# Optimization experiments

Measured on AMD Instinct MI355X. Metric: run time of the kernel, lower is better.

The kernel has to match this reference:

```python
import jax, jax.numpy as jnp
import numpy as np

EPS = 1e-12  # torch F.normalize eps

def _l2norm(v, axis):
    n = jnp.sqrt(jnp.sum(v * v, axis=axis, keepdims=True))
    return v / jnp.maximum(n, EPS)

def setup_inputs() -> dict:
    key = jax.random.key(0)
    k1, k2, k3 = jax.random.split(key, 3)
    B, M, D, K = 32, 2048, 1024, 64
    init_sc = 1.0 / np.sqrt(D)
    x = jax.random.normal(k1, (B, M, D), dtype=jnp.float32)
    W = init_sc * jax.random.normal(k2, (K, D), dtype=jnp.float32)          # fc1.weight
    centroids = init_sc * jax.random.normal(k3, (K, D), dtype=jnp.float32)  # self.centeroids
    return {"x": x, "W": W, "centroids": centroids}

def reference(x, W, centroids):
    # x: [B, M, D] frame features; W, centroids: [K, D]
    x = _l2norm(x, axis=-1)                                   # per-frame L2 normalize
    logits = jnp.einsum('bmd,kd->bmk', x, W)                  # fc1 (no bias)
    a = jax.nn.softmax(logits, axis=-1)                       # soft assignment [B, M, K]
    # vlad[b,k,:] = sum_m a[b,m,k] * (x[b,m,:] - centroids[k,:])
    #            = (A^T X)[b,k,:] - (sum_m a[b,m,k]) * centroids[k,:]
    vlad = jnp.einsum('bmk,bmd->bkd', a, x) - a.sum(axis=1)[..., None] * centroids
    vlad = _l2norm(vlad, axis=-1)                             # intra-normalization per cluster
    v = vlad.reshape(vlad.shape[0], -1)                       # [B, K*D]
    return _l2norm(v, axis=-1)                                # global L2 normalize
```

## Files before the change

### kernel.cpp

```cpp
#include <hip/hip_runtime.h>
#include <math.h>


#define NB 32
#define NM 2048
#define ND 1024
#define NK 64

typedef float f32x4 __attribute__((ext_vector_type(4)));
typedef short s16x4 __attribute__((ext_vector_type(4)));
typedef short s16x8 __attribute__((ext_vector_type(8)));

static constexpr float EPS_ = 1e-12f;

__device__ __forceinline__ short f2bf(float f) {
    union { float f; unsigned u; } v; v.f = f;
    unsigned r = v.u + 0x7fffu + ((v.u >> 16) & 1u);
    return (short)(r >> 16);
}

__global__ __launch_bounds__(256) void nv1_logits_softmax(
    const float* __restrict__ x, const float* __restrict__ W,
    short* __restrict__ aT, float* __restrict__ asum)
{
    const int b = blockIdx.y, mt = blockIdx.x;
    const int tid  = threadIdx.x;
    const int w    = tid >> 6, lane = tid & 63, g = lane >> 4, c = lane & 15;
    const int wm   = w >> 1, wk = w & 1;

    __shared__ union {
        struct { short Xs[64][72]; short Ws[64][72]; } st;
        float Ls[64][68];
    } sm;
    __shared__ float red[64][16];
    __shared__ float inv_l[64];
    __shared__ float asum_l[64];

    f32x4 acc[2][2] = {};
    float sq[4] = {0.f, 0.f, 0.f, 0.f};

    const int sr = tid >> 4;
    const int sc = tid & 15;
    const float* xb = x + ((size_t)b * NM + (size_t)mt * 64) * ND;

    for (int d0 = 0; d0 < ND; d0 += 64) {
        __syncthreads();
        #pragma unroll
        for (int i = 0; i < 4; ++i) {
            const int r = sr + 16 * i;
            const float4 xv = *(const float4*)(xb + (size_t)r * ND + d0 + sc * 4);
            const float4 wv = *(const float4*)(W  + (size_t)r * ND + d0 + sc * 4);
            sq[i] += xv.x*xv.x + xv.y*xv.y + xv.z*xv.z + xv.w*xv.w;
            s16x4 xh, wh;
            xh[0]=f2bf(xv.x); xh[1]=f2bf(xv.y); xh[2]=f2bf(xv.z); xh[3]=f2bf(xv.w);
            wh[0]=f2bf(wv.x); wh[1]=f2bf(wv.y); wh[2]=f2bf(wv.z); wh[3]=f2bf(wv.w);
            *(s16x4*)&sm.st.Xs[r][sc * 4] = xh;
            *(s16x4*)&sm.st.Ws[r][sc * 4] = wh;
        }
        __syncthreads();
        #pragma unroll
        for (int s = 0; s < 2; ++s) {
            s16x8 af[2], bf[2];
            #pragma unroll
            for (int f = 0; f < 2; ++f) {
                af[f] = *(const s16x8*)&sm.st.Xs[wm*32 + f*16 + c][s*32 + g*8];
                bf[f] = *(const s16x8*)&sm.st.Ws[wk*32 + f*16 + c][s*32 + g*8];
            }
            #pragma unroll
            for (int fm = 0; fm < 2; ++fm)
                #pragma unroll
                for (int fk = 0; fk < 2; ++fk)
                    acc[fm][fk] = __builtin_amdgcn_mfma_f32_16x16x32_bf16(
                        af[fm], bf[fk], acc[fm][fk], 0, 0, 0);
        }
    }
    __syncthreads();
    #pragma unroll
    for (int i = 0; i < 4; ++i) red[sr + 16*i][sc] = sq[i];
    #pragma unroll
    for (int fm = 0; fm < 2; ++fm)
        #pragma unroll
        for (int fk = 0; fk < 2; ++fk)
            #pragma unroll
            for (int r = 0; r < 4; ++r)
                sm.Ls[wm*32 + fm*16 + g*4 + r][wk*32 + fk*16 + c] = acc[fm][fk][r];
    __syncthreads();
    if (tid < 64) {
        float s = 0.f;
        #pragma unroll
        for (int i = 0; i < 16; ++i) s += red[tid][i];
        inv_l[tid]  = 1.f / fmaxf(sqrtf(s), EPS_);
        asum_l[tid] = 0.f;
    }
    __syncthreads();

    const int row = tid >> 2, q = tid & 3;
    const float iv = inv_l[row];
    float e[16];
    float mx = -3.0e38f;
    #pragma unroll
    for (int j = 0; j < 16; ++j) { e[j] = sm.Ls[row][q*16 + j] * iv; mx = fmaxf(mx, e[j]); }
    mx = fmaxf(mx, __shfl_xor(mx, 1, 64));
    mx = fmaxf(mx, __shfl_xor(mx, 2, 64));
    float smv = 0.f;
    #pragma unroll
    for (int j = 0; j < 16; ++j) { e[j] = __expf(e[j] - mx); smv += e[j]; }
    smv += __shfl_xor(smv, 1, 64);
    smv += __shfl_xor(smv, 2, 64);
    const float rs = 1.f / smv;
    #pragma unroll
    for (int j = 0; j < 16; ++j) e[j] *= rs;

    alignas(16) short av[16];
    #pragma unroll
    for (int j = 0; j < 16; ++j) av[j] = f2bf(e[j] * iv);
    {
        const size_t base = ((size_t)(b * 32 + mt)) * 4096
                          + (size_t)(q * 16 + (row >> 2)) * 64 + (size_t)(row & 3) * 16;
        *(int4*)(aT + base)     = *(int4*)&av[0];
        *(int4*)(aT + base + 8) = *(int4*)&av[8];
    }
    #pragma unroll
    for (int msk = 4; msk <= 32; msk <<= 1)
        #pragma unroll
        for (int j = 0; j < 16; ++j) e[j] += __shfl_xor(e[j], msk, 64);
    if ((tid & 60) == 0)
        #pragma unroll
        for (int j = 0; j < 16; ++j) atomicAdd(&asum_l[q*16 + j], e[j]);
    __syncthreads();
    if (tid < 64) atomicAdd(asum + b * 64 + tid, asum_l[tid]);
}

__global__ __launch_bounds__(512) void nv2_vlad(
    const float* __restrict__ x, const short* __restrict__ aT,
    const float* __restrict__ asum, const float* __restrict__ cent,
    float* __restrict__ out, float* __restrict__ rowsq)
{
    const int b = blockIdx.y, dt = blockIdx.x;
    const int tid  = threadIdx.x;
    const int w    = tid >> 6, lane = tid & 63, g = lane >> 4, c = lane & 15;
    const int wk   = w >> 2, wd = w & 3;

    __shared__ short Xl[2][8704];
    __shared__ short Al[2][4352];
    __shared__ float rsq_l[64];

    if (tid < 64) rsq_l[tid] = 0.f;

    f32x4 acc[2][2] = {};

    const int mt_ = tid >> 5;
    const int dq  = tid & 31;
    const float* xg = x + (size_t)b * NM * ND + (size_t)dt * 128;

    const uint32_t xbase = (uint32_t)(uintptr_t)&Xl[0][0];
    const uint32_t abase = (uint32_t)(uintptr_t)&Al[0][0];

    float4 xr[4]; int4 ar;

    auto LOAD = [&](int mc) {
        const float* xp = xg + (size_t)mc * 64 * ND;
        #pragma unroll
        for (int i = 0; i < 4; ++i)
            xr[i] = *(const float4*)(xp + (size_t)(mt_ + 16*i) * ND + dq * 4);
        ar = *(const int4*)(aT + ((size_t)(b * 32 + mc)) * 4096 + tid * 8);
    };
    auto WRITE = [&](int p) {
        #pragma unroll
        for (int i = 0; i < 4; ++i) {
            const int m = mt_ + 16 * i;
            s16x4 h;
            h[0]=f2bf(xr[i].x); h[1]=f2bf(xr[i].y); h[2]=f2bf(xr[i].z); h[3]=f2bf(xr[i].w);
            *(s16x4*)&Xl[p][((dq>>2)*16 + (m>>2))*68 + (m&3)*16 + (dq&3)*4] = h;
        }
        const int e0 = tid * 8, idx = e0 >> 6, wo = e0 & 63;
        *(int2*)&Al[p][idx*68 + wo]     = make_int2(ar.x, ar.y);
        *(int2*)&Al[p][idx*68 + wo + 4] = make_int2(ar.z, ar.w);
    };
    auto COMPUTE = [&](int p) {
        const uint32_t xb_ = xbase + (uint32_t)p * 8704u * 2u;
        const uint32_t ab_ = abase + (uint32_t)p * 4352u * 2u;
        s16x4 A[2][2][2], B[2][2][2];
        #pragma unroll
        for (int f = 0; f < 2; ++f)
            #pragma unroll
            for (int s = 0; s < 2; ++s)
                #pragma unroll
                for (int r = 0; r < 2; ++r) {
                    const uint32_t srow = (uint32_t)(s*8 + g*2 + r);
                    const uint32_t aoff = ab_ + (((uint32_t)(wk*2 + f)*16u + srow)*68u)*2u + (uint32_t)c*8u;
                    const uint32_t boff = xb_ + (((uint32_t)(wd*2 + f)*16u + srow)*68u)*2u + (uint32_t)c*8u;
                    asm volatile("ds_read_b64_tr_b16 %0, %1" : "=v"(A[f][s][r]) : "v"(aoff));
                    asm volatile("ds_read_b64_tr_b16 %0, %1" : "=v"(B[f][s][r]) : "v"(boff));
                }
        asm volatile("s_waitcnt lgkmcnt(0)" ::: "memory");
        __builtin_amdgcn_sched_barrier(0);
        #pragma unroll
        for (int s = 0; s < 2; ++s)
            #pragma unroll
            for (int fk = 0; fk < 2; ++fk) {
                const s16x8 af = __builtin_shufflevector(A[fk][s][0], A[fk][s][1], 0,1,2,3,4,5,6,7);
                #pragma unroll
                for (int fd = 0; fd < 2; ++fd) {
                    const s16x8 bf = __builtin_shufflevector(B[fd][s][0], B[fd][s][1], 0,1,2,3,4,5,6,7);
                    acc[fk][fd] = __builtin_amdgcn_mfma_f32_16x16x32_bf16(af, bf, acc[fk][fd], 0, 0, 0);
                }
            }
    };

    LOAD(0); WRITE(0);
    __syncthreads();
    int p = 0;
    for (int mc = 0; mc < 32; ++mc) {
        if (mc < 31) LOAD(mc + 1);
        COMPUTE(p);
        if (mc < 31) WRITE(p ^ 1);
        __syncthreads();
        p ^= 1;
    }

    const float* cb = cent + (size_t)dt * 128;
    #pragma unroll
    for (int fk = 0; fk < 2; ++fk)
        #pragma unroll
        for (int r = 0; r < 4; ++r) {
            const int k = wk*32 + fk*16 + g*4 + r;
            const float as = asum[b * 64 + k];
            float s2 = 0.f;
            #pragma unroll
            for (int fd = 0; fd < 2; ++fd) {
                const int d = wd*32 + fd*16 + c;
                const float v = acc[fk][fd][r] - as * cb[(size_t)k * ND + d];
                out[((size_t)b * 64 + k) * ND + (size_t)dt * 128 + d] = v;
                s2 += v * v;
            }
            s2 += __shfl_xor(s2, 1, 64);
            s2 += __shfl_xor(s2, 2, 64);
            s2 += __shfl_xor(s2, 4, 64);
            s2 += __shfl_xor(s2, 8, 64);
            if (c == 0) atomicAdd(&rsq_l[k], s2);
        }
    __syncthreads();
    if (tid < 64) atomicAdd(rowsq + b * 64 + tid, rsq_l[tid]);
}

__global__ __launch_bounds__(256) void nv3_norm(
    float* __restrict__ out, const float* __restrict__ rowsq)
{
    const int b = blockIdx.y, ck = blockIdx.x;
    const int tid = threadIdx.x;
    __shared__ float rinv[64];
    __shared__ float gred[64];
    __shared__ float ginv_s;
    if (tid < 64) {
        const float rs = rowsq[b * NK + tid];
        const float n  = fmaxf(sqrtf(rs), EPS_);
        rinv[tid] = 1.f / n;
        gred[tid] = (rs / n) / n;
    }
    __syncthreads();
    if (tid == 0) {
        float s = 0.f;
        for (int k = 0; k < 64; ++k) s += gred[k];
        ginv_s = 1.f / fmaxf(sqrtf(s), EPS_);
    }
    __syncthreads();
    const float gi = ginv_s;
    float* ob = out + (size_t)b * (NK * ND);
    #pragma unroll
    for (int it = 0; it < 4; ++it) {
        const int idx = ck * 4096 + it * 1024 + tid * 4;
        const float sc = rinv[idx >> 10] * gi;
        float4 v = *(float4*)(ob + idx);
        v.x *= sc; v.y *= sc; v.z *= sc; v.w *= sc;
        *(float4*)(ob + idx) = v;
    }
}

extern "C" void kernel_launch(void* const* d_in, const int* in_sizes, int n_in,
                              void* d_out, int out_size, void* d_ws, size_t ws_size,
                              hipStream_t stream)
{
    const float* x    = (const float*)d_in[0];
    const float* W    = (const float*)d_in[1];
    const float* cent = (const float*)d_in[2];
    float* out = (float*)d_out;

    short* aT    = (short*)d_ws;
    float* asum  = (float*)((char*)d_ws + (size_t)NB * NM * NK * 2);
    float* rowsq = asum + NB * NK;

    hipMemsetAsync(asum, 0, 2 * NB * NK * sizeof(float), stream);

    nv1_logits_softmax<<<dim3(NM / 64, NB), 256, 0, stream>>>(x, W, aT, asum);
    nv2_vlad<<<dim3(ND / 128, NB), 512, 0, stream>>>(x, aT, asum, cent, out, rowsq);
    nv3_norm<<<dim3(16, NB), 256, 0, stream>>>(out, rowsq);
}
```

Measured before the change: 447.0 us.

## Write pre-tiled bf16 x in logits kernel and stream it via async LDS loads

The softmax kernel now also writes a bf16 copy of x, laid out in the tile order the VLAD kernel consumes. The VLAD kernel reads that copy with global_load_lds directly into shared memory through a triple-buffered pipeline, replacing register staging and fp32-to-bf16 conversion. This halves the bytes the VLAD kernel reads for x but adds an equal-size write to the first kernel and a larger workspace. LDS row padding is removed, which may introduce bank conflicts in the transpose reads.

```diff
diff --git a/kernel.cpp b/kernel.cpp
--- a/kernel.cpp
+++ b/kernel.cpp
@@ -19,9 +19,15 @@
     return (short)(r >> 16);
 }
 
+__device__ __forceinline__ void gload16(const void* g, void* l) {
+    __builtin_amdgcn_global_load_lds(
+        (const __attribute__((address_space(1))) void*)g,
+        (__attribute__((address_space(3))) void*)l, 16, 0, 0);
+}
+
 __global__ __launch_bounds__(256) void nv1_logits_softmax(
     const float* __restrict__ x, const float* __restrict__ W,
-    short* __restrict__ aT, float* __restrict__ asum)
+    short* __restrict__ aT, short* __restrict__ xbT, float* __restrict__ asum)
 {
     const int b = blockIdx.y, mt = blockIdx.x;
     const int tid  = threadIdx.x;
@@ -56,6 +62,12 @@
             wh[0]=f2bf(wv.x); wh[1]=f2bf(wv.y); wh[2]=f2bf(wv.z); wh[3]=f2bf(wv.w);
             *(s16x4*)&sm.st.Xs[r][sc * 4] = xh;
             *(s16x4*)&sm.st.Ws[r][sc * 4] = wh;
+            const int dg   = d0 + sc * 4;
+            const int dt_  = dg >> 7;
+            const int dblk = (dg >> 4) & 7;
+            const size_t gp = (((size_t)(b * 32 + mt) * 8 + dt_) << 13)
+                            + (size_t)((dblk * 16 + (r >> 2)) * 64 + (r & 3) * 16 + (dg & 15));
+            *(s16x4*)(xbT + gp) = xh;
         }
         __syncthreads();
         #pragma unroll
@@ -132,7 +144,7 @@
 }
 
 __global__ __launch_bounds__(512) void nv2_vlad(
-    const float* __restrict__ x, const short* __restrict__ aT,
+    const short* __restrict__ xbT, const short* __restrict__ aT,
     const float* __restrict__ asum, const float* __restrict__ cent,
     float* __restrict__ out, float* __restrict__ rowsq)
 {
@@ -141,45 +153,25 @@
     const int w    = tid >> 6, lane = tid & 63, g = lane >> 4, c = lane & 15;
     const int wk   = w >> 2, wd = w & 3;
 
-    __shared__ short Xl[2][8704];
-    __shared__ short Al[2][4352];
+    __shared__ short Xl[3][8192];
+    __shared__ short Al[3][4096];
     __shared__ float rsq_l[64];
 
     if (tid < 64) rsq_l[tid] = 0.f;
 
     f32x4 acc[2][2] = {};
 
-    const int mt_ = tid >> 5;
-    const int dq  = tid & 31;
-    const float* xg = x + (size_t)b * NM * ND + (size_t)dt * 128;
-
-    const uint32_t xbase = (uint32_t)(uintptr_t)&Xl[0][0];
-    const uint32_t abase = (uint32_t)(uintptr_t)&Al[0][0];
-
-    float4 xr[4]; int4 ar;
-
-    auto LOAD = [&](int mc) {
-        const float* xp = xg + (size_t)mc * 64 * ND;
-        #pragma unroll
-        for (int i = 0; i < 4; ++i)
-            xr[i] = *(const float4*)(xp + (size_t)(mt_ + 16*i) * ND + dq * 4);
-        ar = *(const int4*)(aT + ((size_t)(b * 32 + mc)) * 4096 + tid * 8);
+    auto STAGE = [&](int mc, int p) {
+        const short* xs  = xbT + (((size_t)(b * 32 + mc) * 8 + dt) << 13);
+        const short* as_ = aT  + ((size_t)(b * 32 + mc) << 12);
+        gload16(xs  + w * 1024 + lane * 8,       &Xl[p][w * 1024]);
+        gload16(xs  + w * 1024 + 512 + lane * 8, &Xl[p][w * 1024 + 512]);
+        gload16(as_ + w * 512 + lane * 8,        &Al[p][w * 512]);
     };
-    auto WRITE = [&](int p) {
-        #pragma unroll
-        for (int i = 0; i < 4; ++i) {
-            const int m = mt_ + 16 * i;
-            s16x4 h;
-            h[0]=f2bf(xr[i].x); h[1]=f2bf(xr[i].y); h[2]=f2bf(xr[i].z); h[3]=f2bf(xr[i].w);
-            *(s16x4*)&Xl[p][((dq>>2)*16 + (m>>2))*68 + (m&3)*16 + (dq&3)*4] = h;
-        }
-        const int e0 = tid * 8, idx = e0 >> 6, wo = e0 & 63;
-        *(int2*)&Al[p][idx*68 + wo]     = make_int2(ar.x, ar.y);
-        *(int2*)&Al[p][idx*68 + wo + 4] = make_int2(ar.z, ar.w);
-    };
+
     auto COMPUTE = [&](int p) {
-        const uint32_t xb_ = xbase + (uint32_t)p * 8704u * 2u;
-        const uint32_t ab_ = abase + (uint32_t)p * 4352u * 2u;
+        const uint32_t ab_ = (uint32_t)(uintptr_t)&Al[p][0];
+        const uint32_t xb_ = (uint32_t)(uintptr_t)&Xl[p][0];
         s16x4 A[2][2][2], B[2][2][2];
         #pragma unroll
         for (int f = 0; f < 2; ++f)
@@ -188,8 +180,8 @@
                 #pragma unroll
                 for (int r = 0; r < 2; ++r) {
                     const uint32_t srow = (uint32_t)(s*8 + g*2 + r);
-                    const uint32_t aoff = ab_ + (((uint32_t)(wk*2 + f)*16u + srow)*68u)*2u + (uint32_t)c*8u;
-                    const uint32_t boff = xb_ + (((uint32_t)(wd*2 + f)*16u + srow)*68u)*2u + (uint32_t)c*8u;
+                    const uint32_t aoff = ab_ + (((uint32_t)(wk*2 + f)*16u + srow)*128u) + (uint32_t)c*8u;
+                    const uint32_t boff = xb_ + (((uint32_t)(wd*2 + f)*16u + srow)*128u) + (uint32_t)c*8u;
                     asm volatile("ds_read_b64_tr_b16 %0, %1" : "=v"(A[f][s][r]) : "v"(aoff));
                     asm volatile("ds_read_b64_tr_b16 %0, %1" : "=v"(B[f][s][r]) : "v"(boff));
                 }
@@ -208,15 +200,14 @@
             }
     };
 
-    LOAD(0); WRITE(0);
-    __syncthreads();
-    int p = 0;
+    STAGE(0, 0);
+    STAGE(1, 1);
     for (int mc = 0; mc < 32; ++mc) {
-        if (mc < 31) LOAD(mc + 1);
-        COMPUTE(p);
-        if (mc < 31) WRITE(p ^ 1);
-        __syncthreads();
-        p ^= 1;
+        if (mc < 31) asm volatile("s_waitcnt vmcnt(3)" ::: "memory");
+        else         asm volatile("s_waitcnt vmcnt(0)" ::: "memory");
+        __builtin_amdgcn_s_barrier();
+        if (mc + 2 < 32) STAGE(mc + 2, (mc + 2) % 3);
+        COMPUTE(mc % 3);
     }
 
     const float* cb = cent + (size_t)dt * 128;
@@ -287,12 +278,13 @@
     float* out = (float*)d_out;
 
     short* aT    = (short*)d_ws;
-    float* asum  = (float*)((char*)d_ws + (size_t)NB * NM * NK * 2);
+    short* xbT   = (short*)((char*)d_ws + (size_t)NB * NM * NK * 2);
+    float* asum  = (float*)((char*)d_ws + (size_t)NB * NM * NK * 2 + (size_t)NB * NM * ND * 2);
     float* rowsq = asum + NB * NK;
 
     hipMemsetAsync(asum, 0, 2 * NB * NK * sizeof(float), stream);
 
-    nv1_logits_softmax<<<dim3(NM / 64, NB), 256, 0, stream>>>(x, W, aT, asum);
-    nv2_vlad<<<dim3(ND / 128, NB), 512, 0, stream>>>(x, aT, asum, cent, out, rowsq);
+    nv1_logits_softmax<<<dim3(NM / 64, NB), 256, 0, stream>>>(x, W, aT, xbT, asum);
+    nv2_vlad<<<dim3(ND / 128, NB), 512, 0, stream>>>(xbT, aT, asum, cent, out, rowsq);
     nv3_norm<<<dim3(16, NB), 256, 0, stream>>>(out, rowsq);
 }
```

After: 433.9 us. -2.9%, faster.
